# Performance work log

Hardware: AMD Instinct MI355X
Metric: run time of the kernel (lower is better)

Reference implementation:

```python
import jax, jax.numpy as jnp
import numpy as np

N_ROWS = 4096   # output features (N)
M_COLS = 4096   # input features (M)
BATCH = 4096
NNZ_PER_ROW = 819


def setup_inputs() -> dict:
    rng = np.random.default_rng(0)
    # sample NNZ_PER_ROW distinct, sorted column indices per row (CSR structure)
    cols = np.argsort(rng.random((N_ROWS, M_COLS)), axis=1)[:, :NNZ_PER_ROW]
    cols = np.sort(cols, axis=1).reshape(-1).astype(np.int32)            # [nnz]
    row_ids = np.repeat(np.arange(N_ROWS, dtype=np.int32), NNZ_PER_ROW)  # [nnz], expanded indptr

    key = jax.random.key(0)
    k1, k2, k3 = jax.random.split(key, 3)
    inp = jax.random.normal(k1, (BATCH, M_COLS), dtype=jnp.float32)
    W_val = jax.random.normal(k2, (N_ROWS * NNZ_PER_ROW,), dtype=jnp.float32) * 0.02
    bias = jax.random.normal(k3, (N_ROWS,), dtype=jnp.float32)
    return {
        "input": inp,
        "W_val": W_val,
        "bias": bias,
        "row_ids": jnp.asarray(row_ids),
        "cols": jnp.asarray(cols),
        "N": N_ROWS,
    }


def reference(input, W_val, bias, row_ids, cols, N):
    # Faithful math of SparseLinearFunction: y = x @ W^T + bias where W is the
    # CSR matrix (W_val, row_ids, cols) of shape (N, M). Densify via scatter
    # (CSR has unique (row, col) pairs) then use a single GEMM.
    M = input.shape[-1]
    W = jnp.zeros((N, M), dtype=W_val.dtype).at[row_ids, cols].set(W_val)  # [N, M]
    return jnp.matmul(input, W.T) + bias  # [B, N]
```

## Files before the change

kernel.cpp:

```cpp
#include <hip/hip_runtime.h>
#include <hip/hip_bf16.h>
#include <stdint.h>


#define B_DIM 4096
#define M_DIM 4096
#define N_DIM 4096
#define NNZ_ROW 819

typedef __attribute__((ext_vector_type(8))) __bf16 bf16x8;
typedef __attribute__((ext_vector_type(4))) float f32x4;

__device__ __forceinline__ unsigned short f32_to_bf16(float f) {
    union { float f; unsigned int u; } v;
    v.f = f;
    unsigned int r = v.u + 0x7FFFu + ((v.u >> 16) & 1u);
    return (unsigned short)(r >> 16);
}

__device__ __forceinline__ void load_lds16(const void* g, void* l) {
    __builtin_amdgcn_global_load_lds(
        (const __attribute__((address_space(1))) void*)g,
        (__attribute__((address_space(3))) void*)l,
        16, 0, 0);
}

__global__ __launch_bounds__(256) void densify_w(
    const float* __restrict__ wval,
    const int* __restrict__ cols,
    unsigned short* __restrict__ wb) {
    __shared__ __attribute__((aligned(16))) unsigned short row_s[M_DIM];
    const int row = blockIdx.x;
    const int tid = threadIdx.x;
    uint4* rs4 = (uint4*)row_s;
    rs4[tid]       = make_uint4(0u, 0u, 0u, 0u);
    rs4[tid + 256] = make_uint4(0u, 0u, 0u, 0u);
    __syncthreads();
    const size_t base = (size_t)row * NNZ_ROW;
    for (int j = tid; j < NNZ_ROW; j += 256) {
        const int c = cols[base + j];
        row_s[c] = f32_to_bf16(wval[base + j]);
    }
    __syncthreads();
    uint4* dst = (uint4*)(wb + (size_t)row * M_DIM);
    dst[tid]       = rs4[tid];
    dst[tid + 256] = rs4[tid + 256];
}

__global__ __launch_bounds__(256) void cvt_x_bf16(
    const float4* __restrict__ x, uint4* __restrict__ y, int n8) {
    int i = blockIdx.x * 256 + threadIdx.x;
    if (i >= n8) return;
    const float4 a = x[2 * i];
    const float4 b = x[2 * i + 1];
    union { ushort ush[8]; uint4 u4; } o;
    o.ush[0] = f32_to_bf16(a.x); o.ush[1] = f32_to_bf16(a.y);
    o.ush[2] = f32_to_bf16(a.z); o.ush[3] = f32_to_bf16(a.w);
    o.ush[4] = f32_to_bf16(b.x); o.ush[5] = f32_to_bf16(b.y);
    o.ush[6] = f32_to_bf16(b.z); o.ush[7] = f32_to_bf16(b.w);
    y[i] = o.u4;
}


#define BK 32

__global__ __launch_bounds__(256) void gemm_bt_bias(
    const unsigned short* __restrict__ Xb,
    const unsigned short* __restrict__ Wb,
    const float* __restrict__ bias,
    float* __restrict__ out)
{
    __shared__ __attribute__((aligned(16))) unsigned short As[128 * BK];
    __shared__ __attribute__((aligned(16))) unsigned short Bs[128 * BK];

    const int tid    = threadIdx.x;
    const int wid    = tid >> 6;
    const int lane   = tid & 63;
    const int wm     = wid & 1;
    const int wn     = wid >> 1;
    const int lane15 = lane & 15;
    const int laneq  = lane >> 4;

    const int bm0 = blockIdx.y * 128;
    const int bn0 = blockIdx.x * 128;

    const int srow = (lane >> 2);
    const int skof = ((lane & 3) ^ ((lane >> 3) & 3)) * 8;

    const unsigned short* aSrc0 =
        Xb + (size_t)(bm0 + wid * 16 + srow) * M_DIM + skof;
    const unsigned short* aSrc1 = aSrc0 + (size_t)64 * M_DIM;
    const unsigned short* bSrc0 =
        Wb + (size_t)(bn0 + wid * 16 + srow) * M_DIM + skof;
    const unsigned short* bSrc1 = bSrc0 + (size_t)64 * M_DIM;

    unsigned short* aDst0 = As + wid * 512;
    unsigned short* aDst1 = As + (wid + 4) * 512;
    unsigned short* bDst0 = Bs + wid * 512;
    unsigned short* bDst1 = Bs + (wid + 4) * 512;

    f32x4 acc[4][4];
#pragma unroll
    for (int i = 0; i < 4; ++i)
#pragma unroll
        for (int j = 0; j < 4; ++j) acc[i][j] = (f32x4)0.0f;

    const int slot = (laneq ^ ((lane15 >> 1) & 3)) * 8;
    const unsigned short* aFragP[4];
    const unsigned short* bFragP[4];
#pragma unroll
    for (int t = 0; t < 4; ++t) {
        aFragP[t] = As + (wm * 64 + t * 16 + lane15) * BK + slot;
        bFragP[t] = Bs + (wn * 64 + t * 16 + lane15) * BK + slot;
    }

    for (int kt = 0; kt < M_DIM; kt += BK) {
        load_lds16(aSrc0 + kt, aDst0);
        load_lds16(aSrc1 + kt, aDst1);
        load_lds16(bSrc0 + kt, bDst0);
        load_lds16(bSrc1 + kt, bDst1);
        __syncthreads();

        bf16x8 af[4], bf[4];
#pragma unroll
        for (int t = 0; t < 4; ++t) {
            af[t] = *((const bf16x8*)aFragP[t]);
            bf[t] = *((const bf16x8*)bFragP[t]);
        }
#pragma unroll
        for (int mt = 0; mt < 4; ++mt)
#pragma unroll
            for (int nt = 0; nt < 4; ++nt)
                acc[mt][nt] = __builtin_amdgcn_mfma_f32_16x16x32_bf16(
                    af[mt], bf[nt], acc[mt][nt], 0, 0, 0);
        __syncthreads();
    }

#pragma unroll
    for (int nt = 0; nt < 4; ++nt) {
        const int col = bn0 + wn * 64 + nt * 16 + lane15;
        const float bv = bias[col];
#pragma unroll
        for (int mt = 0; mt < 4; ++mt) {
            const int row0 = bm0 + wm * 64 + mt * 16 + laneq * 4;
#pragma unroll
            for (int r = 0; r < 4; ++r) {
                out[(size_t)(row0 + r) * N_DIM + col] = acc[mt][nt][r] + bv;
            }
        }
    }
}


extern "C" void kernel_launch(void* const* d_in, const int* in_sizes, int n_in,
                              void* d_out, int out_size, void* d_ws, size_t ws_size,
                              hipStream_t stream) {
    const float* x       = (const float*)d_in[0];
    const float* wval    = (const float*)d_in[1];
    const float* bias    = (const float*)d_in[2];
    const int*   cols    = (const int*)d_in[4];
    float* out = (float*)d_out;

    unsigned short* Wb = (unsigned short*)d_ws;
    unsigned short* Xb = Wb + (size_t)N_DIM * M_DIM;

    densify_w<<<dim3(N_DIM), dim3(256), 0, stream>>>(wval, cols, Wb);
    {
        int n8 = (B_DIM * M_DIM) / 8;
        cvt_x_bf16<<<dim3(n8 / 256), dim3(256), 0, stream>>>(
            (const float4*)x, (uint4*)Xb, n8);
    }
    gemm_bt_bias<<<dim3(N_DIM / 128, B_DIM / 128), dim3(256), 0, stream>>>(
        Xb, Wb, bias, out);
}
```

Before: 318.4 us.

## Double-buffer LDS tiles and switch GEMM to 32x32x16 MFMA

The GEMM main loop now double-buffers its A and B LDS tiles, issuing the next K-slice's async global-to-LDS loads before computing the current one, and drops one barrier per iteration. Each wave's 64x64 sub-tile is computed with 2x2 32x32x16 bf16 MFMAs instead of 4x4 16x16x32 ones, which cuts LDS fragment reads per MFMA. Launch bounds now request 4 blocks per SM. The goal is to hide global load latency and raise MFMA throughput, at the cost of twice the LDS and a single barrier that may leave a WAR hazard on the buffer being refilled.

```diff
diff --git a/kernel.cpp b/kernel.cpp
--- a/kernel.cpp
+++ b/kernel.cpp
@@ -7,9 +7,10 @@
 #define M_DIM 4096
 #define N_DIM 4096
 #define NNZ_ROW 819
+#define BK 32
 
 typedef __attribute__((ext_vector_type(8))) __bf16 bf16x8;
-typedef __attribute__((ext_vector_type(4))) float f32x4;
+typedef __attribute__((ext_vector_type(16))) float f32x16;
 
 __device__ __forceinline__ unsigned short f32_to_bf16(float f) {
     union { float f; unsigned int u; } v;
@@ -62,24 +63,22 @@
 }
 
 
-#define BK 32
-
-__global__ __launch_bounds__(256) void gemm_bt_bias(
+__global__ __launch_bounds__(256, 4) void gemm_bt_bias(
     const unsigned short* __restrict__ Xb,
     const unsigned short* __restrict__ Wb,
     const float* __restrict__ bias,
     float* __restrict__ out)
 {
-    __shared__ __attribute__((aligned(16))) unsigned short As[128 * BK];
-    __shared__ __attribute__((aligned(16))) unsigned short Bs[128 * BK];
+    __shared__ __attribute__((aligned(16))) unsigned short As[2 * 128 * BK];
+    __shared__ __attribute__((aligned(16))) unsigned short Bs[2 * 128 * BK];
 
     const int tid    = threadIdx.x;
     const int wid    = tid >> 6;
     const int lane   = tid & 63;
     const int wm     = wid & 1;
     const int wn     = wid >> 1;
-    const int lane15 = lane & 15;
-    const int laneq  = lane >> 4;
+    const int m31    = lane & 31;
+    const int chalf  = lane >> 5;
 
     const int bm0 = blockIdx.y * 128;
     const int bn0 = blockIdx.x * 128;
@@ -94,58 +93,72 @@
         Wb + (size_t)(bn0 + wid * 16 + srow) * M_DIM + skof;
     const unsigned short* bSrc1 = bSrc0 + (size_t)64 * M_DIM;
 
-    unsigned short* aDst0 = As + wid * 512;
-    unsigned short* aDst1 = As + (wid + 4) * 512;
-    unsigned short* bDst0 = Bs + wid * 512;
-    unsigned short* bDst1 = Bs + (wid + 4) * 512;
+    const int dOff0 = wid * 512;
+    const int dOff1 = (wid + 4) * 512;
 
-    f32x4 acc[4][4];
+    const int q2 = (m31 >> 1) & 3;
+    int aOff[2][2], bOff[2][2];
 #pragma unroll
-    for (int i = 0; i < 4; ++i)
+    for (int t = 0; t < 2; ++t)
 #pragma unroll
-        for (int j = 0; j < 4; ++j) acc[i][j] = (f32x4)0.0f;
+        for (int s = 0; s < 2; ++s) {
+            const int slot = ((s * 2 + chalf) ^ q2) * 8;
+            aOff[t][s] = (wm * 64 + t * 32 + m31) * BK + slot;
+            bOff[t][s] = (wn * 64 + t * 32 + m31) * BK + slot;
+        }
 
-    const int slot = (laneq ^ ((lane15 >> 1) & 3)) * 8;
-    const unsigned short* aFragP[4];
-    const unsigned short* bFragP[4];
+    f32x16 acc[2][2];
 #pragma unroll
-    for (int t = 0; t < 4; ++t) {
-        aFragP[t] = As + (wm * 64 + t * 16 + lane15) * BK + slot;
-        bFragP[t] = Bs + (wn * 64 + t * 16 + lane15) * BK + slot;
-    }
+    for (int i = 0; i < 2; ++i)
+#pragma unroll
+        for (int j = 0; j < 2; ++j) acc[i][j] = (f32x16)0.0f;
 
+    load_lds16(aSrc0, As + dOff0);
+    load_lds16(aSrc1, As + dOff1);
+    load_lds16(bSrc0, Bs + dOff0);
+    load_lds16(bSrc1, Bs + dOff1);
+    __syncthreads();
+
+    int buf = 0;
     for (int kt = 0; kt < M_DIM; kt += BK) {
-        load_lds16(aSrc0 + kt, aDst0);
-        load_lds16(aSrc1 + kt, aDst1);
-        load_lds16(bSrc0 + kt, bDst0);
-        load_lds16(bSrc1 + kt, bDst1);
+        const int nbase = (buf ^ 1) * (128 * BK);
+        if (kt + BK < M_DIM) {
+            load_lds16(aSrc0 + kt + BK, As + nbase + dOff0);
+            load_lds16(aSrc1 + kt + BK, As + nbase + dOff1);
+            load_lds16(bSrc0 + kt + BK, Bs + nbase + dOff0);
+            load_lds16(bSrc1 + kt + BK, Bs + nbase + dOff1);
+        }
+        const int cbase = buf * (128 * BK);
+#pragma unroll
+        for (int s = 0; s < 2; ++s) {
+            bf16x8 af[2], bf[2];
+#pragma unroll
+            for (int t = 0; t < 2; ++t) {
+                af[t] = *((const bf16x8*)(As + cbase + aOff[t][s]));
+                bf[t] = *((const bf16x8*)(Bs + cbase + bOff[t][s]));
+            }
+#pragma unroll
+            for (int mt = 0; mt < 2; ++mt)
+#pragma unroll
+                for (int nt = 0; nt < 2; ++nt)
+                    acc[mt][nt] = __builtin_amdgcn_mfma_f32_32x32x16_bf16(
+                        af[mt], bf[nt], acc[mt][nt], 0, 0, 0);
+        }
         __syncthreads();
-
-        bf16x8 af[4], bf[4];
-#pragma unroll
-        for (int t = 0; t < 4; ++t) {
-            af[t] = *((const bf16x8*)aFragP[t]);
-            bf[t] = *((const bf16x8*)bFragP[t]);
-        }
-#pragma unroll
-        for (int mt = 0; mt < 4; ++mt)
-#pragma unroll
-            for (int nt = 0; nt < 4; ++nt)
-                acc[mt][nt] = __builtin_amdgcn_mfma_f32_16x16x32_bf16(
-                    af[mt], bf[nt], acc[mt][nt], 0, 0, 0);
-        __syncthreads();
+        buf ^= 1;
     }
 
 #pragma unroll
-    for (int nt = 0; nt < 4; ++nt) {
-        const int col = bn0 + wn * 64 + nt * 16 + lane15;
+    for (int nt = 0; nt < 2; ++nt) {
+        const int col = bn0 + wn * 64 + nt * 32 + m31;
         const float bv = bias[col];
 #pragma unroll
-        for (int mt = 0; mt < 4; ++mt) {
-            const int row0 = bm0 + wm * 64 + mt * 16 + laneq * 4;
+        for (int mt = 0; mt < 2; ++mt) {
+            const int row_base = bm0 + wm * 64 + mt * 32 + 4 * chalf;
 #pragma unroll
-            for (int r = 0; r < 4; ++r) {
-                out[(size_t)(row0 + r) * N_DIM + col] = acc[mt][nt][r] + bv;
+            for (int r = 0; r < 16; ++r) {
+                const int row = row_base + (r & 3) + 8 * (r >> 2);
+                out[(size_t)row * N_DIM + col] = acc[mt][nt][r] + bv;
             }
         }
     }
```

New measurement: 305.9 us. 3.9% less time.

## Double-buffer LDS tiles in GEMM to overlap global loads with MFMA

Applied to the files above, without the earlier changes.

Doubles the LDS A/B tile buffers and prefetches the next K-tile with global_load_lds while the current tile feeds the MFMAs, so each iteration needs one barrier instead of two. The aim is to hide global-to-LDS latency behind compute. It also raises launch_bounds to request 4 blocks per CU. The extra LDS use is modest at 32 KB per block. The risk is that the single barrier may not guarantee the async LDS loads have completed, since the compiler's vmcnt waits are relied on at the syncthreads.

```diff
diff --git a/kernel.cpp b/kernel.cpp
--- a/kernel.cpp
+++ b/kernel.cpp
@@ -7,6 +7,7 @@
 #define M_DIM 4096
 #define N_DIM 4096
 #define NNZ_ROW 819
+#define BK 32
 
 typedef __attribute__((ext_vector_type(8))) __bf16 bf16x8;
 typedef __attribute__((ext_vector_type(4))) float f32x4;
@@ -62,16 +63,14 @@
 }
 
 
-#define BK 32
-
-__global__ __launch_bounds__(256) void gemm_bt_bias(
+__global__ __launch_bounds__(256, 4) void gemm_bt_bias(
     const unsigned short* __restrict__ Xb,
     const unsigned short* __restrict__ Wb,
     const float* __restrict__ bias,
     float* __restrict__ out)
 {
-    __shared__ __attribute__((aligned(16))) unsigned short As[128 * BK];
-    __shared__ __attribute__((aligned(16))) unsigned short Bs[128 * BK];
+    __shared__ __attribute__((aligned(16))) unsigned short As[2 * 128 * BK];
+    __shared__ __attribute__((aligned(16))) unsigned short Bs[2 * 128 * BK];
 
     const int tid    = threadIdx.x;
     const int wid    = tid >> 6;
@@ -94,10 +93,16 @@
         Wb + (size_t)(bn0 + wid * 16 + srow) * M_DIM + skof;
     const unsigned short* bSrc1 = bSrc0 + (size_t)64 * M_DIM;
 
-    unsigned short* aDst0 = As + wid * 512;
-    unsigned short* aDst1 = As + (wid + 4) * 512;
-    unsigned short* bDst0 = Bs + wid * 512;
-    unsigned short* bDst1 = Bs + (wid + 4) * 512;
+    const int dOff0 = wid * 512;
+    const int dOff1 = (wid + 4) * 512;
+
+    const int slot = (laneq ^ ((lane15 >> 1) & 3)) * 8;
+    int aOff[4], bOff[4];
+#pragma unroll
+    for (int t = 0; t < 4; ++t) {
+        aOff[t] = (wm * 64 + t * 16 + lane15) * BK + slot;
+        bOff[t] = (wn * 64 + t * 16 + lane15) * BK + slot;
+    }
 
     f32x4 acc[4][4];
 #pragma unroll
@@ -105,27 +110,28 @@
 #pragma unroll
         for (int j = 0; j < 4; ++j) acc[i][j] = (f32x4)0.0f;
 
-    const int slot = (laneq ^ ((lane15 >> 1) & 3)) * 8;
-    const unsigned short* aFragP[4];
-    const unsigned short* bFragP[4];
-#pragma unroll
-    for (int t = 0; t < 4; ++t) {
-        aFragP[t] = As + (wm * 64 + t * 16 + lane15) * BK + slot;
-        bFragP[t] = Bs + (wn * 64 + t * 16 + lane15) * BK + slot;
-    }
+    load_lds16(aSrc0, As + dOff0);
+    load_lds16(aSrc1, As + dOff1);
+    load_lds16(bSrc0, Bs + dOff0);
+    load_lds16(bSrc1, Bs + dOff1);
+    __syncthreads();
 
+    int buf = 0;
     for (int kt = 0; kt < M_DIM; kt += BK) {
-        load_lds16(aSrc0 + kt, aDst0);
-        load_lds16(aSrc1 + kt, aDst1);
-        load_lds16(bSrc0 + kt, bDst0);
-        load_lds16(bSrc1 + kt, bDst1);
-        __syncthreads();
+        const int nbase = (buf ^ 1) * (128 * BK);
+        if (kt + BK < M_DIM) {
+            load_lds16(aSrc0 + kt + BK, As + nbase + dOff0);
+            load_lds16(aSrc1 + kt + BK, As + nbase + dOff1);
+            load_lds16(bSrc0 + kt + BK, Bs + nbase + dOff0);
+            load_lds16(bSrc1 + kt + BK, Bs + nbase + dOff1);
+        }
+        const int cbase = buf * (128 * BK);
 
         bf16x8 af[4], bf[4];
 #pragma unroll
         for (int t = 0; t < 4; ++t) {
-            af[t] = *((const bf16x8*)aFragP[t]);
-            bf[t] = *((const bf16x8*)bFragP[t]);
+            af[t] = *((const bf16x8*)(As + cbase + aOff[t]));
+            bf[t] = *((const bf16x8*)(Bs + cbase + bOff[t]));
         }
 #pragma unroll
         for (int mt = 0; mt < 4; ++mt)
@@ -133,7 +139,9 @@
             for (int nt = 0; nt < 4; ++nt)
                 acc[mt][nt] = __builtin_amdgcn_mfma_f32_16x16x32_bf16(
                     af[mt], bf[nt], acc[mt][nt], 0, 0, 0);
+
         __syncthreads();
+        buf ^= 1;
     }
 
 #pragma unroll
```

New measurement: 302.5 us. 1.05x faster.
